# Optimization experiments

Hardware: AMD Instinct MI355X
Metric: run time of the kernel (lower is better)

## Reference

```python
import jax, jax.numpy as jnp
import numpy as np

# Static config (matches init_kwargs)
DIM, HEADS = 192, 6
PL, LAT, LON = 8, 96, 180
WP, WL, WW = 2, 6, 12          # window size (pressure, lat, lon)
SP, SL, SW = 1, 3, 6           # shift size
N = WP * WL * WW               # tokens per window = 144
NPL, NLAT, NLON = PL // WP, LAT // WL, LON // WW   # 4, 16, 15
NW = NPL * NLAT                # type_of_windows = 64 (lat/pl-dependent bias)
HD = DIM // HEADS              # 32
L = PL * LAT * LON
BIAS_LEN = (2 * WW - 1) * WL * WL * WP * WP   # 3312
EPS = 1e-5


def _position_index():
    # Earth-specific relative position index (Pangu): absolute-position
    # dependence along pressure and latitude, relative along longitude.
    zi = np.arange(WP); zj = -np.arange(WP) * WP
    hi = np.arange(WL); hj = -np.arange(WL) * WL
    w = np.arange(WW)
    c1 = np.stack(np.meshgrid(zi, hi, w, indexing='ij')).reshape(3, -1)
    c2 = np.stack(np.meshgrid(zj, hj, w, indexing='ij')).reshape(3, -1)
    c = (c1[:, :, None] - c2[:, None, :]).transpose(1, 2, 0).copy()
    c[:, :, 2] += WW - 1
    c[:, :, 1] *= 2 * WW - 1
    c[:, :, 0] *= (2 * WW - 1) * WL * WL
    return c.sum(-1)  # (N, N) in [0, BIAS_LEN)


def _attn_mask():
    # Shifted-window mask: lon is periodic on the globe (roll only), so
    # masking is applied along pressure and latitude boundaries only.
    img = np.zeros((1, PL, LAT, LON, 1), np.float32)
    cnt = 0
    for pl in (slice(0, -WP), slice(-WP, -SP), slice(-SP, None)):
        for la in (slice(0, -WL), slice(-WL, -SL), slice(-SL, None)):
            img[:, pl, la, :, :] = cnt
            cnt += 1
    mw = img.reshape(1, NPL, WP, NLAT, WL, NLON, WW, 1)
    mw = mw.transpose(0, 5, 1, 3, 2, 4, 6, 7).reshape(NLON, NW, N)
    am = mw[:, :, None, :] - mw[:, :, :, None]
    return np.where(am != 0, -100.0, 0.0).astype(np.float32)  # (NLON, NW, N, N)


POS_IDX = jnp.asarray(_position_index())
ATTN_MASK = jnp.asarray(_attn_mask())


def layer_norm(x, g, b):
    m = x.mean(-1, keepdims=True)
    v = ((x - m) ** 2).mean(-1, keepdims=True)
    return (x - m) * jax.lax.rsqrt(v + EPS) * g + b


def setup_inputs() -> dict:
    key = jax.random.key(0)
    ks = jax.random.split(key, 10)
    s = 0.02
    return {
        'x': jax.random.normal(ks[0], (1, L, DIM), jnp.float32),
        'norm1_g': jnp.ones((DIM,), jnp.float32),
        'norm1_b': jnp.zeros((DIM,), jnp.float32),
        'qkv_w': jax.random.normal(ks[1], (DIM, 3 * DIM), jnp.float32) * s,
        'qkv_b': jnp.zeros((3 * DIM,), jnp.float32),
        'earth_bias': jax.random.normal(ks[2], (BIAS_LEN, NW, HEADS), jnp.float32) * s,
        'proj_w': jax.random.normal(ks[3], (DIM, DIM), jnp.float32) * s,
        'proj_b': jnp.zeros((DIM,), jnp.float32),
        'norm2_g': jnp.ones((DIM,), jnp.float32),
        'norm2_b': jnp.zeros((DIM,), jnp.float32),
        'fc1_w': jax.random.normal(ks[4], (DIM, 4 * DIM), jnp.float32) * s,
        'fc1_b': jnp.zeros((4 * DIM,), jnp.float32),
        'fc2_w': jax.random.normal(ks[5], (4 * DIM, DIM), jnp.float32) * s,
        'fc2_b': jnp.zeros((DIM,), jnp.float32),
    }


def reference(x, norm1_g, norm1_b, qkv_w, qkv_b, earth_bias, proj_w, proj_b,
              norm2_g, norm2_b, fc1_w, fc1_b, fc2_w, fc2_b):
    B, Ltok, C = x.shape
    shortcut = x
    h = layer_norm(x, norm1_g, norm1_b).reshape(B, PL, LAT, LON, C)
    # shifted windows (lon is periodic -> plain roll)
    h = jnp.roll(h, shift=(-SP, -SL, -SW), axis=(1, 2, 3))
    # window partition -> (B*NLON, NW, N, C); lon windows folded into batch
    xw = h.reshape(B, NPL, WP, NLAT, WL, NLON, WW, C)
    xw = xw.transpose(0, 5, 1, 3, 2, 4, 6, 7).reshape(B * NLON, NW, N, C)
    # earth-specific attention
    qkv = (xw @ qkv_w + qkv_b).reshape(B * NLON, NW, N, 3, HEADS, HD)
    qkv = qkv.transpose(3, 0, 1, 4, 2, 5)  # (3, B_, NW, H, N, HD)
    q, k, v = qkv[0], qkv[1], qkv[2]
    attn = jnp.einsum('bwhnd,bwhmd->bwhnm', q * (HD ** -0.5), k)
    bias = earth_bias[POS_IDX].reshape(N, N, NW, HEADS).transpose(2, 3, 0, 1)
    attn = attn + bias[None]                        # (B_, NW, H, N, N)
    attn = attn.reshape(B, NLON, NW, HEADS, N, N) + ATTN_MASK[None, :, :, None]
    attn = jax.nn.softmax(attn.reshape(B * NLON, NW, HEADS, N, N), axis=-1)
    out = jnp.einsum('bwhnm,bwhmd->bwhnd', attn, v)
    out = out.transpose(0, 1, 3, 2, 4).reshape(B * NLON, NW, N, C)
    out = out @ proj_w + proj_b
    # window reverse + roll back
    h = out.reshape(B, NLON, NPL, NLAT, WP, WL, WW, C)
    h = h.transpose(0, 2, 4, 3, 5, 1, 6, 7).reshape(B, PL, LAT, LON, C)
    h = jnp.roll(h, shift=(SP, SL, SW), axis=(1, 2, 3)).reshape(B, Ltok, C)
    x = shortcut + h
    # MLP block (GELU exact, as nn.GELU default)
    y = layer_norm(x, norm2_g, norm2_b)
    y = jax.nn.gelu(y @ fc1_w + fc1_b, approximate=False) @ fc2_w + fc2_b
    return x + y
```

## Files before the change

kernel.cpp:

```cpp
#include <hip/hip_runtime.h>
#include <hip/hip_bf16.h>
#include <math.h>

typedef unsigned short u16;
typedef __attribute__((ext_vector_type(8))) short short8;
typedef __attribute__((ext_vector_type(4))) short short4v;
typedef __attribute__((ext_vector_type(4))) float f32x4;

#define MFMA(a,b,c) __builtin_amdgcn_mfma_f32_16x16x32_bf16(a,b,c,0,0,0)
#define DIM 192

__device__ __forceinline__ float bf2f(u16 u){ unsigned v=((unsigned)u)<<16; float f; __builtin_memcpy(&f,&v,4); return f; }
__device__ __forceinline__ u16 f2bf(float f){ unsigned v; __builtin_memcpy(&v,&f,4); v = v + 0x7fffu + ((v>>16)&1u); return (u16)(v>>16); }

__device__ __forceinline__ void gl_lds16(const u16* g, u16* l){
  __builtin_amdgcn_global_load_lds((const __attribute__((address_space(1))) unsigned int*)g,
                                   (__attribute__((address_space(3))) unsigned int*)l, 16, 0, 0);
}

__device__ __forceinline__ int win_to_tok(int r){
  int lon = r/9216; int rem = r - lon*9216;
  int w = rem/144, n = rem - w*144;
  int ip=w>>4, il=w&15;
  int wp=n/72, t=n-wp*72, wl=t/12, ww=t-wl*12;
  int p=ip*2+wp, la=il*6+wl, lo=lon*12+ww;
  int p0=p+1;  if(p0>=8)   p0-=8;
  int la0=la+3; if(la0>=96) la0-=96;
  int lo0=lo+6; if(lo0>=180)lo0-=180;
  return (p0*96+la0)*180+lo0;
}

__global__ __launch_bounds__(256) void ln1_window_kernel(
    const float* __restrict__ x, const float* __restrict__ g, const float* __restrict__ b,
    u16* __restrict__ A)
{
  int r = blockIdx.x*4 + (threadIdx.x>>6);
  int lane = threadIdx.x & 63;
  size_t src = (size_t)win_to_tok(r)*DIM;
  float v0=x[src+lane], v1=x[src+64+lane], v2=x[src+128+lane];
  float s=v0+v1+v2;
  for(int m=32;m>=1;m>>=1) s += __shfl_xor(s,m);
  float mean = s*(1.f/192.f);
  float d0=v0-mean,d1=v1-mean,d2=v2-mean;
  float q=d0*d0+d1*d1+d2*d2;
  for(int m=32;m>=1;m>>=1) q += __shfl_xor(q,m);
  float rstd = rsqrtf(q*(1.f/192.f)+1e-5f);
  size_t o = (size_t)r*DIM;
  A[o+lane]     = f2bf(d0*rstd*g[lane]     + b[lane]);
  A[o+64+lane]  = f2bf(d1*rstd*g[64+lane]  + b[64+lane]);
  A[o+128+lane] = f2bf(d2*rstd*g[128+lane] + b[128+lane]);
}

__global__ __launch_bounds__(256) void transpose_bf16_kernel(
    const float* __restrict__ src, u16* __restrict__ dst, int K, int N)
{
  int idx = blockIdx.x*256 + threadIdx.x;
  if (idx >= K*N) return;
  int k = idx / N, n = idx - k*N;
  dst[n*K + k] = f2bf(src[idx]);
}

__global__ __launch_bounds__(256) void pf_w1_kernel(const float* __restrict__ fc1w, u16* __restrict__ W1f){
  int idx = blockIdx.x*256 + threadIdx.x;
  int e = idx & 7, g3 = idx >> 3;
  int g = g3 % 24, r3 = g3 / 24;
  int r = r3 & 31, hc = r3 >> 5;
  int k = ((g ^ (r&7))<<3) + e;
  W1f[idx] = f2bf(fc1w[(size_t)k*768 + hc*32 + r]);
}
__global__ __launch_bounds__(256) void pf_w2_kernel(const float* __restrict__ fc2w, u16* __restrict__ W2f){
  int idx = blockIdx.x*256 + threadIdx.x;
  int e = idx & 7, g3 = idx >> 3;
  int g = g3 & 3, r3 = g3 >> 2;
  int r = r3 % 192, hc = r3 / 192;
  int k = hc*32 + ((g ^ (r&3))<<3) + e;
  W2f[idx] = f2bf(fc2w[(size_t)k*192 + r]);
}

__global__ __launch_bounds__(256) void bias_expand_kernel(
    const float* __restrict__ eb, u16* __restrict__ B2)
{
  __shared__ int t1s[144], t2s[144], rgs[144];
  __shared__ float ebs[3312];
  int bid = blockIdx.x;
  int w = bid / 6;
  int tid = threadIdx.x;
  if (tid < 144) {
    int n = tid;
    int wp=n/72, t=n-wp*72, wl=t/12, ww=t-wl*12;
    t1s[n] = wp*828 + wl*23 + ww;
    t2s[n] = 1656*wp + 138*wl - ww + 11;
    int ip = w>>4, il = w&15;
    int p = ip*2+wp, la = il*6+wl;
    int rp = (p<6)?0:((p<7)?1:2);
    int rl = (la<90)?0:((la<93)?1:2);
    rgs[n] = rp*3+rl;
  }
  for (int i = tid; i < 3312; i += 256) ebs[i] = eb[(size_t)i*384 + bid];
  __syncthreads();
  size_t ob = (size_t)bid*20736;
  for (int idx = tid; idx < 20736; idx += 256) {
    int i = idx & 3, lane = (idx>>2)&63, t = idx>>8;
    int mt = t%9, nt = t/9;
    int n = nt*16 + (lane&15);
    int m = mt*16 + ((lane>>4)<<2) + i;
    float bv = ebs[t1s[n]+t2s[m]];
    bv += (rgs[n]==rgs[m]) ? 0.f : -100.f;
    B2[ob + idx] = f2bf(bv);
  }
}

#define SM_WS   0
#define SM_QS   36864
#define SM_KS   48384
#define SM_VS   59904
#define SM_PS   0
#define SMEM3   70656

__global__ __launch_bounds__(576) void attn_kernel(
    const u16* __restrict__ A,
    const u16* __restrict__ Wt,
    const float* __restrict__ qkvb,
    const u16* __restrict__ Bexp,
    u16* __restrict__ O)
{
  extern __shared__ char smem[];
  u16* Ws = (u16*)(smem + SM_WS);
  u16* qs = (u16*)(smem + SM_QS);
  u16* ks_= (u16*)(smem + SM_KS);
  u16* vs = (u16*)(smem + SM_VS);
  u16* Ps = (u16*)(smem + SM_PS);

  int bid = blockIdx.x;
  int logical = (bid & 7)*720 + (bid >> 3);
  int lon = logical % 15;
  int wh  = logical / 15;
  int h = wh % 6, w = wh / 6;
  int tid = threadIdx.x, lane = tid & 63, wv = tid >> 6;

  {
    int rr = tid % 96, chunk = tid / 96;
    int mat = rr >> 5, c = rr & 31;
    const u16* s = Wt + (size_t)(mat*192 + h*32 + c)*192 + chunk*32;
    uint4 t0 = *(const uint4*)(s);
    uint4 t1 = *(const uint4*)(s+8);
    uint4 t2 = *(const uint4*)(s+16);
    uint4 t3 = *(const uint4*)(s+24);
    u16* d = Ws + rr*192;
    int r7 = rr & 7, g0 = chunk*4;
    *(uint4*)(d + ((g0  )^r7)*8) = t0;
    *(uint4*)(d + ((g0+1)^r7)*8) = t1;
    *(uint4*)(d + ((g0+2)^r7)*8) = t2;
    *(uint4*)(d + ((g0+3)^r7)*8) = t3;
  }
  if (tid < 512) { int c = tid>>4; vs[c*168 + 144 + (tid&15)] = 0; }
  __syncthreads();

  size_t winbase = (size_t)(lon*64 + w)*144;
  int r0 = wv*16;
  int l15 = lane & 15, lg = lane >> 4;
  int sw7 = l15 & 7;

  short8 af[6];
  {
    const u16* arow = A + (winbase + r0 + l15)*DIM + 8*lg;
    #pragma unroll
    for (int k0=0;k0<6;k0++) af[k0] = *(const short8*)(arow + k0*32);
  }
  const float qscale = 0.17677669529663687f;

  #pragma unroll
  for (int mt=0; mt<2; mt++) {
    f32x4 acc = {0.f,0.f,0.f,0.f};
    const u16* wrow = Ws + (mt*16 + l15)*192;
    #pragma unroll
    for (int k0=0;k0<6;k0++) acc = MFMA(*(const short8*)(wrow + ((k0*4+lg)^sw7)*8), af[k0], acc);
    short4v pk;
    #pragma unroll
    for (int i=0;i<4;i++) pk[i] = (short)f2bf((acc[i] + qkvb[h*32 + mt*16 + 4*lg + i])*qscale);
    *(short4v*)(qs + (r0 + l15)*40 + mt*16 + 4*lg) = pk;
  }
  #pragma unroll
  for (int mt=0; mt<2; mt++) {
    f32x4 acc = {0.f,0.f,0.f,0.f};
    const u16* wrow = Ws + (32 + mt*16 + l15)*192;
    #pragma unroll
    for (int k0=0;k0<6;k0++) acc = MFMA(*(const short8*)(wrow + ((k0*4+lg)^sw7)*8), af[k0], acc);
    short4v pk;
    #pragma unroll
    for (int i=0;i<4;i++) pk[i] = (short)f2bf(acc[i] + qkvb[192 + h*32 + mt*16 + 4*lg + i]);
    *(short4v*)(ks_ + (r0 + l15)*40 + mt*16 + 4*lg) = pk;
  }
  #pragma unroll
  for (int ct=0; ct<2; ct++) {
    f32x4 acc = {0.f,0.f,0.f,0.f};
    const u16* wrow = Ws + (64 + ct*16 + l15)*192;
    #pragma unroll
    for (int k0=0;k0<6;k0++) acc = MFMA(af[k0], *(const short8*)(wrow + ((k0*4+lg)^sw7)*8), acc);
    float bias = qkvb[384 + h*32 + ct*16 + l15];
    short4v pk;
    #pragma unroll
    for (int i=0;i<4;i++) pk[i] = (short)f2bf(acc[i] + bias);
    *(short4v*)(vs + (ct*16 + l15)*168 + r0 + 4*lg) = pk;
  }
  __syncthreads();

  short8 bq = *(const short8*)(qs + (r0 + l15)*40 + 8*lg);
  f32x4 sa[9];
  #pragma unroll
  for (int mt=0; mt<9; mt++) {
    f32x4 z = {0.f,0.f,0.f,0.f};
    sa[mt] = MFMA(*(const short8*)(ks_ + (mt*16 + l15)*40 + 8*lg), bq, z);
  }
  __syncthreads();

  {
    const u16* bb = Bexp + (((size_t)wh*9 + wv)*9)*256 + lane*4;
    #pragma unroll
    for (int mt=0; mt<9; mt++) {
      short4v pk = *(const short4v*)(bb + mt*256);
      #pragma unroll
      for (int i=0;i<4;i++) sa[mt][i] += bf2f((u16)pk[i]);
    }
  }
  float rsum = 0.f;
  #pragma unroll
  for (int mt=0; mt<9; mt++)
    #pragma unroll
    for (int i=0;i<4;i++) { float e = __expf(sa[mt][i]); sa[mt][i] = e; rsum += e; }
  rsum += __shfl_xor(rsum, 16);
  rsum += __shfl_xor(rsum, 32);
  float rinv = 1.f / rsum;
  #pragma unroll
  for (int mt=0; mt<9; mt++) {
    short4v pk;
    #pragma unroll
    for (int i=0;i<4;i++) pk[i] = (short)f2bf(sa[mt][i]);
    *(short4v*)(Ps + (r0 + l15)*168 + mt*16 + 4*lg) = pk;
  }
  {
    short4v z = {0,0,0,0};
    *(short4v*)(Ps + (r0 + l15)*168 + 144 + 4*lg) = z;
  }

  #pragma unroll
  for (int ct2=0; ct2<2; ct2++) {
    f32x4 acc = {0.f,0.f,0.f,0.f};
    const u16* vr = vs + (ct2*16 + l15)*168 + 8*lg;
    const u16* pr = Ps + (r0 + l15)*168 + 8*lg;
    #pragma unroll
    for (int k0=0;k0<5;k0++) acc = MFMA(*(const short8*)(vr + 32*k0), *(const short8*)(pr + 32*k0), acc);
    short4v pk;
    #pragma unroll
    for (int i=0;i<4;i++) pk[i] = (short)f2bf(acc[i]*rinv);
    *(short4v*)(O + (winbase + r0 + l15)*DIM + h*32 + ct2*16 + 4*lg) = pk;
  }
}

#define SMEMP (73728 + 512)
__global__ __launch_bounds__(512, 4) void proj_ln2_kernel(
    const u16* __restrict__ AT,
    const u16* __restrict__ Pw,
    const float* __restrict__ pb, const float* __restrict__ x,
    const float* __restrict__ n2g, const float* __restrict__ n2b,
    float* __restrict__ out, u16* __restrict__ Y)
{
  extern __shared__ char smem[];
  u16* Pws = (u16*)smem;
  int* tokmap = (int*)(smem + 73728);
  int tid = threadIdx.x;
  size_t rbase = (size_t)blockIdx.x*128;
  #pragma unroll
  for (int j=0;j<9;j++){
    int g = j*512 + tid;
    int row = g/24, jj = g - row*24;
    uint4 t = *(const uint4*)(Pw + (size_t)row*192 + jj*8);
    *(uint4*)(Pws + row*192 + ((jj ^ (row&7))*8)) = t;
  }
  if (tid < 128) tokmap[tid] = win_to_tok((int)rbase + tid);
  __syncthreads();

  int lane = tid&63, wv = tid>>6, r0 = wv*16;
  int l15 = lane&15, lg = lane>>4;
  short8 af[6];
  const u16* arow = AT + (rbase + r0 + l15)*DIM + 8*lg;
  #pragma unroll
  for (int k0=0;k0<6;k0++) af[k0] = *(const short8*)(arow + k0*32);

  f32x4 acc[12];
  #pragma unroll
  for (int ct=0; ct<12; ct++) {
    f32x4 a = {0.f,0.f,0.f,0.f};
    const u16* wr = Pws + (ct*16+l15)*192;
    #pragma unroll
    for (int k0=0;k0<6;k0++) a = MFMA(af[k0], *(const short8*)(wr + (((k0*4+lg)^(l15&7))*8)), a);
    acc[ct] = a;
  }
  int toks[4];
  #pragma unroll
  for (int i=0;i<4;i++) toks[i] = tokmap[r0 + 4*lg + i];
  #pragma unroll
  for (int ct=0; ct<12; ct++) {
    int col = ct*16+l15;
    float bias = pb[col];
    #pragma unroll
    for (int i=0;i<4;i++){
      size_t o = (size_t)toks[i]*DIM + col;
      float v = x[o] + acc[ct][i] + bias;
      out[o] = v;
      acc[ct][i] = v;
    }
  }
  float s[4] = {0,0,0,0};
  #pragma unroll
  for (int ct=0; ct<12; ct++) for (int i=0;i<4;i++) s[i] += acc[ct][i];
  #pragma unroll
  for (int i=0;i<4;i++){ for (int m=1;m<16;m<<=1) s[i] += __shfl_xor(s[i], m, 16); s[i] *= (1.f/192.f); }
  float q[4] = {0,0,0,0};
  #pragma unroll
  for (int ct=0; ct<12; ct++) for (int i=0;i<4;i++){ float d = acc[ct][i]-s[i]; q[i] += d*d; }
  #pragma unroll
  for (int i=0;i<4;i++){ for (int m=1;m<16;m<<=1) q[i] += __shfl_xor(q[i], m, 16); q[i] = rsqrtf(q[i]*(1.f/192.f)+1e-5f); }
  #pragma unroll
  for (int ct=0; ct<12; ct++) {
    int col = ct*16+l15;
    float gg = n2g[col], bb = n2b[col];
    #pragma unroll
    for (int i=0;i<4;i++)
      Y[(size_t)toks[i]*DIM + col] = f2bf((acc[ct][i]-s[i])*q[i]*gg + bb);
  }
}

#define SMEM5 69632
__global__ __launch_bounds__(1024, 4) void mlp_kernel(
    const u16* __restrict__ Y,
    const u16* __restrict__ W1f,
    const float* __restrict__ b1,
    const u16* __restrict__ W2f,
    const float* __restrict__ b2,
    float* __restrict__ out)
{
  extern __shared__ char smem[];
  u16* W1b0 = (u16*)smem;
  u16* W1b1 = (u16*)(smem + 12288);
  u16* W2b0 = (u16*)(smem + 24576);
  u16* W2b1 = (u16*)(smem + 36864);
  u16* Hs   = (u16*)(smem + 49152);
  int tid = threadIdx.x;
  size_t rbase = (size_t)blockIdx.x*256;
  int lane = tid&63, wv = tid>>6, r0 = wv*16;
  int l15 = lane&15, lg = lane>>4;

  short8 af[6];
  {
    const u16* yrow = Y + (rbase + r0 + l15)*DIM + 8*lg;
    #pragma unroll
    for (int k0=0;k0<6;k0++) af[k0] = *(const short8*)(yrow + k0*32);
  }

  if (tid < 768) {
    gl_lds16(W1f + (size_t)tid*8, W1b0 + tid*8);
    gl_lds16(W2f + (size_t)tid*8, W2b0 + tid*8);
    gl_lds16(W1f + 6144 + (size_t)tid*8, W1b1 + tid*8);
    gl_lds16(W2f + 6144 + (size_t)tid*8, W2b1 + tid*8);
  }
  __syncthreads();

  f32x4 acc2[12];
  #pragma unroll
  for (int i=0;i<12;i++) acc2[i] = (f32x4){0.f,0.f,0.f,0.f};

  const float GA = -1.5957691216057307f;
  const float GB = -0.07135481627272283f;

  for (int hc=0; hc<24; hc++) {
    u16* B1w = (hc&1) ? W1b1 : W1b0;
    u16* B2w = (hc&1) ? W2b1 : W2b0;
    #pragma unroll
    for (int ct=0; ct<2; ct++) {
      f32x4 a1 = {0.f,0.f,0.f,0.f};
      const u16* wr = B1w + (ct*16+l15)*192;
      #pragma unroll
      for (int k0=0;k0<6;k0++) a1 = MFMA(af[k0], *(const short8*)(wr + (((k0*4+lg)^(l15&7))*8)), a1);
      float bb = b1[hc*32 + ct*16 + l15];
      #pragma unroll
      for (int i=0;i<4;i++){
        float v = a1[i] + bb;
        float t = v*v;
        float m = fmaf(t, GB, GA);
        float e = __expf(v*m);
        float hgl = v*__builtin_amdgcn_rcpf(1.f + e);
        Hs[(r0 + 4*lg + i)*40 + ct*16 + l15] = f2bf(hgl);
      }
    }
    {
      short8 ah = *(const short8*)(Hs + (r0+l15)*40 + 8*lg);
      #pragma unroll
      for (int ct2=0; ct2<12; ct2++) {
        const u16* wr2 = B2w + (ct2*16+l15)*32 + ((lg ^ (l15&3))*8);
        acc2[ct2] = MFMA(ah, *(const short8*)(wr2), acc2[ct2]);
      }
    }
    __syncthreads();
    if (hc < 22 && tid < 768) {
      const u16* s1 = W1f + (size_t)(hc+2)*6144;
      const u16* s2 = W2f + (size_t)(hc+2)*6144;
      u16* d1 = (hc&1) ? W1b1 : W1b0;
      u16* d2 = (hc&1) ? W2b1 : W2b0;
      gl_lds16(s1 + (size_t)tid*8, d1 + tid*8);
      gl_lds16(s2 + (size_t)tid*8, d2 + tid*8);
    }
  }
  #pragma unroll
  for (int ct2=0; ct2<12; ct2++) {
    int col = ct2*16+l15;
    float bb = b2[col];
    #pragma unroll
    for (int i=0;i<4;i++){
      size_t o = (rbase + r0 + 4*lg + i)*DIM + col;
      out[o] = out[o] + acc2[ct2][i] + bb;
    }
  }
}

extern "C" void kernel_launch(void* const* d_in, const int* in_sizes, int n_in,
                              void* d_out, int out_size, void* d_ws, size_t ws_size,
                              hipStream_t stream) {
  const float* x    = (const float*)d_in[0];
  const float* n1g  = (const float*)d_in[1];
  const float* n1b  = (const float*)d_in[2];
  const float* qkvw = (const float*)d_in[3];
  const float* qkvb = (const float*)d_in[4];
  const float* eb   = (const float*)d_in[5];
  const float* projw= (const float*)d_in[6];
  const float* projb= (const float*)d_in[7];
  const float* n2g  = (const float*)d_in[8];
  const float* n2b  = (const float*)d_in[9];
  const float* fc1w = (const float*)d_in[10];
  const float* fc1b = (const float*)d_in[11];
  const float* fc2w = (const float*)d_in[12];
  const float* fc2b = (const float*)d_in[13];
  float* out = (float*)d_out;
  char* ws = (char*)d_ws;

  u16* A   = (u16*)(ws);
  u16* AT  = (u16*)(ws + 53084160);
  u16* Wq  = (u16*)(ws + 106168320);
  u16* Pw  = (u16*)(ws + 106389504);
  u16* W1f = (u16*)(ws + 106463232);
  u16* W2f = (u16*)(ws + 106758144);
  u16* Bexp = (u16*)d_out;

  hipFuncSetAttribute((const void*)attn_kernel,     hipFuncAttributeMaxDynamicSharedMemorySize, SMEM3);
  hipFuncSetAttribute((const void*)proj_ln2_kernel, hipFuncAttributeMaxDynamicSharedMemorySize, SMEMP);
  hipFuncSetAttribute((const void*)mlp_kernel,      hipFuncAttributeMaxDynamicSharedMemorySize, SMEM5);

  transpose_bf16_kernel<<<432, 256, 0, stream>>>(qkvw, Wq, 192, 576);
  transpose_bf16_kernel<<<144, 256, 0, stream>>>(projw, Pw, 192, 192);
  pf_w1_kernel<<<576, 256, 0, stream>>>(fc1w, W1f);
  pf_w2_kernel<<<576, 256, 0, stream>>>(fc2w, W2f);
  bias_expand_kernel<<<384, 256, 0, stream>>>(eb, Bexp);
  ln1_window_kernel<<<34560, 256, 0, stream>>>(x, n1g, n1b, A);
  attn_kernel<<<5760, 576, SMEM3, stream>>>(A, Wq, qkvb, Bexp, AT);
  proj_ln2_kernel<<<1080, 512, SMEMP, stream>>>(AT, Pw, projb, x, n2g, n2b, out, A);
  mlp_kernel<<<540, 1024, SMEM5, stream>>>(A, W1f, fc1b, W2f, fc2b, out);
}
```

Measured before the change: 483.4 us.

## Rewrite MLP kernel with 32x32 MFMA tiles and 64-wide hidden chunks

```diff
diff --git a/kernel.cpp b/kernel.cpp
--- a/kernel.cpp
+++ b/kernel.cpp
@@ -6,8 +6,10 @@
 typedef __attribute__((ext_vector_type(8))) short short8;
 typedef __attribute__((ext_vector_type(4))) short short4v;
 typedef __attribute__((ext_vector_type(4))) float f32x4;
-
-#define MFMA(a,b,c) __builtin_amdgcn_mfma_f32_16x16x32_bf16(a,b,c,0,0,0)
+typedef __attribute__((ext_vector_type(16))) float f32x16;
+
+#define MFMA(a,b,c)   __builtin_amdgcn_mfma_f32_16x16x32_bf16(a,b,c,0,0,0)
+#define MFMA32(a,b,c) __builtin_amdgcn_mfma_f32_32x32x16_bf16(a,b,c,0,0,0)
 #define DIM 192
 
 __device__ __forceinline__ float bf2f(u16 u){ unsigned v=((unsigned)u)<<16; float f; __builtin_memcpy(&f,&v,4); return f; }
@@ -68,13 +70,13 @@
   int k = ((g ^ (r&7))<<3) + e;
   W1f[idx] = f2bf(fc1w[(size_t)k*768 + hc*32 + r]);
 }
-__global__ __launch_bounds__(256) void pf_w2_kernel(const float* __restrict__ fc2w, u16* __restrict__ W2f){
+__global__ __launch_bounds__(256) void pf_w2_kernel(const float* __restrict__ fc2w, u16* __restrict__ W2g){
   int idx = blockIdx.x*256 + threadIdx.x;
-  int e = idx & 7, g3 = idx >> 3;
-  int g = g3 & 3, r3 = g3 >> 2;
-  int r = r3 % 192, hc = r3 / 192;
-  int k = hc*32 + ((g ^ (r&3))<<3) + e;
-  W2f[idx] = f2bf(fc2w[(size_t)k*192 + r]);
+  int e = idx & 7, t = idx >> 3;
+  int p = t & 7; t >>= 3;
+  int oc = t % 192, ck = t / 192;
+  int k = ck*64 + ((p ^ (oc&7))<<3) + e;
+  W2g[idx] = f2bf(fc2w[(size_t)k*192 + oc]);
 }
 
 __global__ __launch_bounds__(256) void bias_expand_kernel(
@@ -259,8 +261,7 @@
 
 #define SMEMP (73728 + 512)
 __global__ __launch_bounds__(512, 4) void proj_ln2_kernel(
-    const u16* __restrict__ AT,
-    const u16* __restrict__ Pw,
+    const u16* __restrict__ AT, const u16* __restrict__ Pw,
     const float* __restrict__ pb, const float* __restrict__ x,
     const float* __restrict__ n2g, const float* __restrict__ n2b,
     float* __restrict__ out, u16* __restrict__ Y)
@@ -331,94 +332,104 @@
   }
 }
 
-#define SMEM5 69632
-__global__ __launch_bounds__(1024, 4) void mlp_kernel(
+#define SMEM5 67584
+__global__ __launch_bounds__(512, 4) void mlp_kernel(
     const u16* __restrict__ Y,
     const u16* __restrict__ W1f,
     const float* __restrict__ b1,
-    const u16* __restrict__ W2f,
+    const u16* __restrict__ W2g,
     const float* __restrict__ b2,
     float* __restrict__ out)
 {
   extern __shared__ char smem[];
-  u16* W1b0 = (u16*)smem;
-  u16* W1b1 = (u16*)(smem + 12288);
-  u16* W2b0 = (u16*)(smem + 24576);
-  u16* W2b1 = (u16*)(smem + 36864);
-  u16* Hs   = (u16*)(smem + 49152);
+  u16* W1b = (u16*)smem;
+  u16* W2b = (u16*)(smem + 24576);
+  u16* Hs  = (u16*)(smem + 49152);
   int tid = threadIdx.x;
-  size_t rbase = (size_t)blockIdx.x*256;
-  int lane = tid&63, wv = tid>>6, r0 = wv*16;
-  int l15 = lane&15, lg = lane>>4;
-
-  short8 af[6];
-  {
-    const u16* yrow = Y + (rbase + r0 + l15)*DIM + 8*lg;
-    #pragma unroll
-    for (int k0=0;k0<6;k0++) af[k0] = *(const short8*)(yrow + k0*32);
-  }
-
-  if (tid < 768) {
-    gl_lds16(W1f + (size_t)tid*8, W1b0 + tid*8);
-    gl_lds16(W2f + (size_t)tid*8, W2b0 + tid*8);
-    gl_lds16(W1f + 6144 + (size_t)tid*8, W1b1 + tid*8);
-    gl_lds16(W2f + 6144 + (size_t)tid*8, W2b1 + tid*8);
-  }
-  __syncthreads();
-
-  f32x4 acc2[12];
-  #pragma unroll
-  for (int i=0;i<12;i++) acc2[i] = (f32x4){0.f,0.f,0.f,0.f};
-
+  size_t rbase = (size_t)blockIdx.x*128;
+  int lane = tid & 63;
+  int l31 = lane & 31, hi = lane >> 5;
+  int wv = tid >> 6;
+  int rg = wv >> 1, ch = wv & 1;
+  int sw7 = l31 & 7;
+
+  gl_lds16(W1f + (size_t)tid*8,          W1b + tid*8);
+  gl_lds16(W1f + (size_t)(512+tid)*8,    W1b + (512+tid)*8);
+  gl_lds16(W1f + (size_t)(1024+tid)*8,   W1b + (1024+tid)*8);
+  gl_lds16(W2g + (size_t)tid*8,          W2b + tid*8);
+  gl_lds16(W2g + (size_t)(512+tid)*8,    W2b + (512+tid)*8);
+  gl_lds16(W2g + (size_t)(1024+tid)*8,   W2b + (1024+tid)*8);
+  __syncthreads();
+
+  f32x16 acc2[3];
+  #pragma unroll
+  for (int t=0;t<3;t++) acc2[t] = (f32x16){0.f,0.f,0.f,0.f,0.f,0.f,0.f,0.f,0.f,0.f,0.f,0.f,0.f,0.f,0.f,0.f};
+
+  const u16* yrow = Y + (rbase + 32*rg + l31)*DIM;
   const float GA = -1.5957691216057307f;
   const float GB = -0.07135481627272283f;
 
-  for (int hc=0; hc<24; hc++) {
-    u16* B1w = (hc&1) ? W1b1 : W1b0;
-    u16* B2w = (hc&1) ? W2b1 : W2b0;
-    #pragma unroll
-    for (int ct=0; ct<2; ct++) {
-      f32x4 a1 = {0.f,0.f,0.f,0.f};
-      const u16* wr = B1w + (ct*16+l15)*192;
+  for (int c = 0; c < 12; ++c) {
+    f32x16 a1 = (f32x16){0.f,0.f,0.f,0.f,0.f,0.f,0.f,0.f,0.f,0.f,0.f,0.f,0.f,0.f,0.f,0.f};
+    #pragma unroll
+    for (int half=0; half<2; ++half) {
+      short8 afr[6];
       #pragma unroll
-      for (int k0=0;k0<6;k0++) a1 = MFMA(af[k0], *(const short8*)(wr + (((k0*4+lg)^(l15&7))*8)), a1);
-      float bb = b1[hc*32 + ct*16 + l15];
+      for (int j=0;j<6;j++) afr[j] = *(const short8*)(yrow + (half*6+j)*16 + 8*hi);
       #pragma unroll
-      for (int i=0;i<4;i++){
-        float v = a1[i] + bb;
+      for (int j=0;j<6;j++) {
+        int gk = 2*(half*6+j) + hi;
+        const u16* wr = W1b + (ch*32 + l31)*192 + ((gk ^ sw7)*8);
+        a1 = MFMA32(afr[j], *(const short8*)wr, a1);
+      }
+    }
+    {
+      float bb = b1[c*64 + 32*ch + l31];
+      #pragma unroll
+      for (int r=0;r<16;r++){
+        float v = a1[r] + bb;
         float t = v*v;
         float m = fmaf(t, GB, GA);
         float e = __expf(v*m);
         float hgl = v*__builtin_amdgcn_rcpf(1.f + e);
-        Hs[(r0 + 4*lg + i)*40 + ct*16 + l15] = f2bf(hgl);
+        int rowf = (r&3) + 8*(r>>2) + 4*hi;
+        Hs[(32*rg + rowf)*72 + 32*ch + l31] = f2bf(hgl);
       }
     }
-    {
-      short8 ah = *(const short8*)(Hs + (r0+l15)*40 + 8*lg);
+    __syncthreads();
+    if (c < 11) {
+      const u16* s1 = W1f + (size_t)(c+1)*12288;
+      gl_lds16(s1 + (size_t)tid*8,        W1b + tid*8);
+      gl_lds16(s1 + (size_t)(512+tid)*8,  W1b + (512+tid)*8);
+      gl_lds16(s1 + (size_t)(1024+tid)*8, W1b + (1024+tid)*8);
+    }
+    #pragma unroll
+    for (int ks=0; ks<4; ++ks) {
+      short8 ah = *(const short8*)(Hs + (32*rg + l31)*72 + ks*16 + 8*hi);
       #pragma unroll
-      for (int ct2=0; ct2<12; ct2++) {
-        const u16* wr2 = B2w + (ct2*16+l15)*32 + ((lg ^ (l15&3))*8);
-        acc2[ct2] = MFMA(ah, *(const short8*)(wr2), acc2[ct2]);
+      for (int t=0;t<3;t++){
+        int oc = 96*ch + 32*t + l31;
+        const u16* wr2 = W2b + oc*64 + (((2*ks+hi) ^ sw7)*8);
+        acc2[t] = MFMA32(ah, *(const short8*)(wr2), acc2[t]);
       }
     }
     __syncthreads();
-    if (hc < 22 && tid < 768) {
-      const u16* s1 = W1f + (size_t)(hc+2)*6144;
-      const u16* s2 = W2f + (size_t)(hc+2)*6144;
-      u16* d1 = (hc&1) ? W1b1 : W1b0;
-      u16* d2 = (hc&1) ? W2b1 : W2b0;
-      gl_lds16(s1 + (size_t)tid*8, d1 + tid*8);
-      gl_lds16(s2 + (size_t)tid*8, d2 + tid*8);
-    }
-  }
-  #pragma unroll
-  for (int ct2=0; ct2<12; ct2++) {
-    int col = ct2*16+l15;
+    if (c < 11) {
+      const u16* s2 = W2g + (size_t)(c+1)*12288;
+      gl_lds16(s2 + (size_t)tid*8,        W2b + tid*8);
+      gl_lds16(s2 + (size_t)(512+tid)*8,  W2b + (512+tid)*8);
+      gl_lds16(s2 + (size_t)(1024+tid)*8, W2b + (1024+tid)*8);
+    }
+  }
+  #pragma unroll
+  for (int t=0;t<3;t++){
+    int col = 96*ch + 32*t + l31;
     float bb = b2[col];
     #pragma unroll
-    for (int i=0;i<4;i++){
-      size_t o = (rbase + r0 + 4*lg + i)*DIM + col;
-      out[o] = out[o] + acc2[ct2][i] + bb;
+    for (int r=0;r<16;r++){
+      int row = 32*rg + (r&3) + 8*(r>>2) + 4*hi;
+      size_t o = (rbase + row)*DIM + col;
+      out[o] = out[o] + acc2[t][r] + bb;
     }
   }
 }
@@ -448,7 +459,7 @@
   u16* Wq  = (u16*)(ws + 106168320);
   u16* Pw  = (u16*)(ws + 106389504);
   u16* W1f = (u16*)(ws + 106463232);
-  u16* W2f = (u16*)(ws + 106758144);
+  u16* W2g = (u16*)(ws + 106758144);
   u16* Bexp = (u16*)d_out;
 
   hipFuncSetAttribute((const void*)attn_kernel,     hipFuncAttributeMaxDynamicSharedMemorySize, SMEM3);
@@ -458,10 +469,10 @@
   transpose_bf16_kernel<<<432, 256, 0, stream>>>(qkvw, Wq, 192, 576);
   transpose_bf16_kernel<<<144, 256, 0, stream>>>(projw, Pw, 192, 192);
   pf_w1_kernel<<<576, 256, 0, stream>>>(fc1w, W1f);
-  pf_w2_kernel<<<576, 256, 0, stream>>>(fc2w, W2f);
+  pf_w2_kernel<<<576, 256, 0, stream>>>(fc2w, W2g);
   bias_expand_kernel<<<384, 256, 0, stream>>>(eb, Bexp);
   ln1_window_kernel<<<34560, 256, 0, stream>>>(x, n1g, n1b, A);
   attn_kernel<<<5760, 576, SMEM3, stream>>>(A, Wq, qkvb, Bexp, AT);
   proj_ln2_kernel<<<1080, 512, SMEMP, stream>>>(AT, Pw, projb, x, n2g, n2b, out, A);
-  mlp_kernel<<<540, 1024, SMEM5, stream>>>(A, W1f, fc1b, W2f, fc2b, out);
-}
+  mlp_kernel<<<1080, 512, SMEM5, stream>>>(A, W1f, fc1b, W2g, fc2b, out);
+}
```

After: 508.5 us. 1.05x slower.
